# Performance work log

Hardware: AMD Instinct MI355X
Metric: run time of the kernel (lower is better)

Reference implementation:

```python
import jax, jax.numpy as jnp
import numpy as np

C = 512

def conv1x1(x, w, b):
    # x: [B,C,H,W], w: [O,C], b: [O]
    return jnp.einsum('bchw,oc->bohw', x, w) + b[None, :, None, None]

def setup_inputs() -> dict:
    key = jax.random.key(0)
    ks = jax.random.split(key, 7)
    s = 1.0 / np.sqrt(C)
    x = jax.random.normal(ks[0], (8, C, 64, 64), dtype=jnp.float32)
    wq = jax.random.uniform(ks[1], (C, C), jnp.float32, -s, s)
    bq = jax.random.uniform(ks[2], (C,), jnp.float32, -s, s)
    wk = jax.random.uniform(ks[3], (C, C), jnp.float32, -s, s)
    bk = jax.random.uniform(ks[4], (C,), jnp.float32, -s, s)
    wv = jax.random.uniform(ks[5], (C, C), jnp.float32, -s, s)
    bv = jax.random.uniform(ks[6], (C,), jnp.float32, -s, s)
    return {"x": x, "wq": wq, "bq": bq, "wk": wk, "bk": bk, "wv": wv, "bv": bv}

def reference(x, wq, bq, wk, bk, wv, bv):
    B, Cc, H, W = x.shape
    q = conv1x1(x, wq, bq).reshape(B, Cc, H * W)   # [B,C,N]
    k = conv1x1(x, wk, bk).reshape(B, Cc, H * W)   # [B,C,N]
    v = conv1x1(x, wv, bv).reshape(B, Cc, H * W)   # [B,C,N]
    attn = jnp.einsum('bcn,bdn->bcd', q, k)        # q @ k^T over spatial dim -> [B,C,C]
    attn = jax.nn.softmax(attn, axis=-1)
    out = jnp.einsum('bcd,bdn->bcn', attn, v).reshape(B, Cc, H, W)
    return out + x
```

## Files before the change

### kernel.cpp

```cpp
#include <hip/hip_runtime.h>
#include <cstdint>

typedef unsigned short u16;
typedef unsigned int   u32;
typedef _Float16 f16;

typedef __attribute__((ext_vector_type(8))) _Float16 f16x8;
typedef __attribute__((ext_vector_type(4))) float    f32x4;

__device__ __forceinline__ u16 f2h(float f) {
    union { f16 h; u16 u; } c; c.h = (f16)f; return c.u;
}
__device__ __forceinline__ float h2f(u16 u) {
    union { u16 u; f16 h; } c; c.u = u; return (float)c.h;
}

__device__ __forceinline__ void async_copy16(const u16* g, u16* lds) {
    __builtin_amdgcn_global_load_lds(
        (const __attribute__((address_space(1))) void*)g,
        (__attribute__((address_space(3))) void*)lds,
        16, 0, 0);
}

__device__ __forceinline__ void gemm_nt_f16(
    u16* smem, const u16* __restrict__ A, int lda,
    const u16* __restrict__ B, int ldb, int K, f32x4 acc[4][4])
{
    u16* As = smem; u16* Bs = smem + 4096;
    const int t = threadIdx.x, w = t >> 6, lane = t & 63;
    const int srow = lane >> 2;
    const int skc  = (((lane & 3) ^ ((lane >> 3) & 3)) * 8);
    const int ra0 = (w*2+0)*16 + srow, ra1 = (w*2+1)*16 + srow;
    const u16* gA0 = A + (size_t)ra0 * lda + skc;
    const u16* gA1 = A + (size_t)ra1 * lda + skc;
    const u16* gB0 = B + (size_t)ra0 * ldb + skc;
    const u16* gB1 = B + (size_t)ra1 * ldb + skc;
    u16* lA0 = As + (w*2+0)*512; u16* lA1 = As + (w*2+1)*512;
    u16* lB0 = Bs + (w*2+0)*512; u16* lB1 = Bs + (w*2+1)*512;
    const int fr = lane & 15, fq = lane >> 4;
    const int fc = (fq ^ ((fr >> 1) & 3)) * 8;
    const int wm = (w >> 1) * 64, wn = (w & 1) * 64;
    const u16* fA = As + (wm + fr) * 32 + fc;
    const u16* fB = Bs + (wn + fr) * 32 + fc;

    for (int k0 = 0; k0 < K; k0 += 32) {
        async_copy16(gA0 + k0, lA0);
        async_copy16(gA1 + k0, lA1);
        async_copy16(gB0 + k0, lB0);
        async_copy16(gB1 + k0, lB1);
        __syncthreads();
        f16x8 af[4], bf[4];
#pragma unroll
        for (int i = 0; i < 4; i++) af[i] = *(const f16x8*)(fA + i * 512);
#pragma unroll
        for (int i = 0; i < 4; i++) bf[i] = *(const f16x8*)(fB + i * 512);
#pragma unroll
        for (int mi = 0; mi < 4; mi++)
#pragma unroll
            for (int ni = 0; ni < 4; ni++)
                acc[mi][ni] = __builtin_amdgcn_mfma_f32_16x16x32_f16(
                    af[mi], bf[ni], acc[mi][ni], 0, 0, 0);
        __syncthreads();
    }
}

__device__ __forceinline__ void zero_acc(f32x4 acc[4][4]) {
#pragma unroll
    for (int i = 0; i < 4; i++)
#pragma unroll
        for (int j = 0; j < 4; j++) {
            f32x4 z = {0.f, 0.f, 0.f, 0.f};
            acc[i][j] = z;
        }
}

__global__ __launch_bounds__(256) void k_convw(const float* __restrict__ wq,
                                               const float* __restrict__ wk,
                                               u16* __restrict__ Wq2,
                                               u16* __restrict__ Wkh,
                                               float* __restrict__ s)
{
    const int t = blockIdx.x * 256 + threadIdx.x;
    if (t < 4096) s[t] = 0.f;
    const int e = t * 4;
    const int sel = e >> 18;
    const int off = e & 262143;
    const float* src = sel ? wk : wq;
    float4 v = *(const float4*)(src + off);
    ushort4 h;
    h.x = f2h(v.x); h.y = f2h(v.y); h.z = f2h(v.z); h.w = f2h(v.w);
    if (sel == 0) {
        int i = off >> 9, c = off & 511;
        *(ushort4*)(Wq2 + (size_t)i * 1024 + c) = h;
        *(ushort4*)(Wq2 + (size_t)i * 1024 + 512 + c) = h;
    } else {
        *(ushort4*)(Wkh + off) = h;
    }
}

__global__ __launch_bounds__(256) void k_wvt(const float* __restrict__ wv,
                                             u16* __restrict__ WvT)
{
    __shared__ u16 tile[64][70];
    const int t = threadIdx.x;
    const int d0 = blockIdx.y * 64;
    const int c0 = blockIdx.x * 64;
    const int rr = t >> 4, col4 = (t & 15) * 4;
#pragma unroll
    for (int i = 0; i < 4; i++) {
        int row = i * 16 + rr;
        float4 v = *(const float4*)(wv + (size_t)(d0 + row) * 512 + c0 + col4);
        ushort4 h;
        h.x = f2h(v.x); h.y = f2h(v.y); h.z = f2h(v.z); h.w = f2h(v.w);
        *(ushort4*)&tile[row][col4] = h;
    }
    __syncthreads();
#pragma unroll
    for (int i = 0; i < 4; i++) {
        int crow = i * 16 + rr;
        ushort4 o;
        o.x = tile[col4 + 0][crow];
        o.y = tile[col4 + 1][crow];
        o.z = tile[col4 + 2][crow];
        o.w = tile[col4 + 3][crow];
        *(ushort4*)(WvT + (size_t)(c0 + crow) * 512 + d0 + col4) = o;
    }
}

__global__ __launch_bounds__(256) void k_convx(const float* __restrict__ x,
                                               u16* __restrict__ Xh,
                                               u16* __restrict__ XT,
                                               float* __restrict__ s)
{
    __shared__ u16 tile[64][70];
    const int t  = threadIdx.x;
    const int b  = blockIdx.z;
    const int c0 = blockIdx.y * 64;
    const int n0 = blockIdx.x * 64;
    const int rr   = t >> 4;
    const int col4 = (t & 15) * 4;

    const float* src = x + ((size_t)b * 512 + c0) * 4096 + n0;
    u16* xh = Xh + ((size_t)b * 512 + c0) * 4096 + n0;
#pragma unroll
    for (int i = 0; i < 4; i++) {
        int row = i * 16 + rr;
        float4 v = *(const float4*)(src + (size_t)row * 4096 + col4);
        ushort4 h;
        h.x = f2h(v.x); h.y = f2h(v.y); h.z = f2h(v.z); h.w = f2h(v.w);
        *(ushort4*)&tile[row][col4] = h;
        *(ushort4*)(xh + (size_t)row * 4096 + col4) = h;
        float p = v.x + v.y + v.z + v.w;
        p += __shfl_xor(p, 1); p += __shfl_xor(p, 2);
        p += __shfl_xor(p, 4); p += __shfl_xor(p, 8);
        if ((t & 15) == 0) atomicAdd(&s[b * 512 + c0 + row], p);
    }
    __syncthreads();
    u16* dst = XT + ((size_t)b * 4096 + n0) * 512 + c0;
#pragma unroll
    for (int i = 0; i < 4; i++) {
        int nrow = i * 16 + rr;
        ushort4 o;
        o.x = tile[col4 + 0][nrow];
        o.y = tile[col4 + 1][nrow];
        o.z = tile[col4 + 2][nrow];
        o.w = tile[col4 + 3][nrow];
        *(ushort4*)(dst + (size_t)nrow * 512 + col4) = o;
    }
}

__global__ __launch_bounds__(256) void k_gram(const u16* __restrict__ Xh,
                                              float* __restrict__ Gp)
{
    __shared__ u16 smem[8192];
    const int n0 = blockIdx.x * 128;
    const int m0 = blockIdx.y * 128;
    const int bz = blockIdx.z;
    const int b  = bz >> 2, ks = bz & 3;

    const u16* Ap = Xh + (size_t)b * 512 * 4096 + (size_t)m0 * 4096 + ks * 1024;
    const u16* Bp = Xh + (size_t)b * 512 * 4096 + (size_t)n0 * 4096 + ks * 1024;

    f32x4 acc[4][4];
    zero_acc(acc);
    gemm_nt_f16(smem, Ap, 4096, Bp, 4096, 1024, acc);

    const int t = threadIdx.x, w = t >> 6, lane = t & 63;
    const int wm = (w >> 1) * 64, wn = (w & 1) * 64;
    const int cn = lane & 15, cq = lane >> 4;

    float* outp = Gp + ((size_t)(ks * 8 + b) * 512 + m0) * 512 + n0;
#pragma unroll
    for (int mi = 0; mi < 4; mi++)
#pragma unroll
        for (int ni = 0; ni < 4; ni++)
#pragma unroll
            for (int r = 0; r < 4; r++) {
                int m = wm + mi * 16 + cq * 4 + r;
                int n = wn + ni * 16 + cn;
                outp[(size_t)m * 512 + n] = acc[mi][ni][r];
            }
}

__global__ __launch_bounds__(256) void k_gred(const float* __restrict__ Gp,
                                              u16* __restrict__ Ghl)
{
    const size_t idx = ((size_t)blockIdx.x * 256 + threadIdx.x) * 4;
    const size_t st = (size_t)8 * 512 * 512;
    float4 g0 = *(const float4*)(Gp + idx);
    float4 g1 = *(const float4*)(Gp + idx + st);
    float4 g2 = *(const float4*)(Gp + idx + 2 * st);
    float4 g3 = *(const float4*)(Gp + idx + 3 * st);
    float gx = g0.x + g1.x + g2.x + g3.x;
    float gy = g0.y + g1.y + g2.y + g3.y;
    float gz = g0.z + g1.z + g2.z + g3.z;
    float gw = g0.w + g1.w + g2.w + g3.w;
    ushort4 hi, lo;
    hi.x = f2h(gx); lo.x = f2h(gx - h2f(hi.x));
    hi.y = f2h(gy); lo.y = f2h(gy - h2f(hi.y));
    hi.z = f2h(gz); lo.z = f2h(gz - h2f(hi.z));
    hi.w = f2h(gw); lo.w = f2h(gw - h2f(hi.w));
    const size_t row = idx >> 9;
    const int c = (int)(idx & 511);
    *(ushort4*)(Ghl + row * 1024 + c) = hi;
    *(ushort4*)(Ghl + row * 1024 + 512 + c) = lo;
}

__global__ __launch_bounds__(256) void k_uv(const float* __restrict__ wq,
                                            const float* __restrict__ bq,
                                            const float* __restrict__ wk,
                                            const float* __restrict__ s,
                                            float* __restrict__ ubar,
                                            float* __restrict__ vv)
{
    const int b = blockIdx.y;
    const int which = blockIdx.x >> 3;
    const int r0 = (blockIdx.x & 7) * 64;
    const int t = threadIdx.x;
    const int i = r0 + (t >> 2), l4 = t & 3;
    const float* W = which ? wk : wq;
    const float* sb = s + b * 512;
    float acc = 0.f;
#pragma unroll 4
    for (int k = 0; k < 32; k++) {
        int c = k * 16 + l4 * 4;
        float4 w4 = *(const float4*)(W + (size_t)i * 512 + c);
        float4 s4 = *(const float4*)(sb + c);
        acc += w4.x * s4.x + w4.y * s4.y + w4.z * s4.z + w4.w * s4.w;
    }
    acc += __shfl_xor(acc, 1);
    acc += __shfl_xor(acc, 2);
    if (l4 == 0) {
        if (which) vv[b * 512 + i] = acc;
        else       ubar[b * 512 + i] = acc + 4096.0f * bq[i];
    }
}

__global__ __launch_bounds__(256) void k_T(const u16* __restrict__ Wq2,
                                           const u16* __restrict__ Ghl,
                                           u16* __restrict__ Tb)
{
    __shared__ u16 smem[8192];
    const int n0 = blockIdx.x * 128;
    const int m0 = blockIdx.y * 128;
    const int b  = blockIdx.z;

    const u16* Ap = Wq2 + (size_t)m0 * 1024;
    const u16* Bp = Ghl + (size_t)b * 512 * 1024 + (size_t)n0 * 1024;

    f32x4 acc[4][4];
    zero_acc(acc);
    gemm_nt_f16(smem, Ap, 1024, Bp, 1024, 1024, acc);

    const int t = threadIdx.x, w = t >> 6, lane = t & 63;
    const int wm = (w >> 1) * 64, wn = (w & 1) * 64;
    const int cn = lane & 15, cq = lane >> 4;

    u16* outp = Tb + ((size_t)b * 512 + m0) * 512 + n0;
#pragma unroll
    for (int mi = 0; mi < 4; mi++)
#pragma unroll
        for (int ni = 0; ni < 4; ni++)
#pragma unroll
            for (int r = 0; r < 4; r++) {
                int m = wm + mi * 16 + cq * 4 + r;
                int n = wn + ni * 16 + cn;
                outp[(size_t)m * 512 + n] = f2h(acc[mi][ni][r]);
            }
}

__global__ __launch_bounds__(256) void k_S(
    const u16* __restrict__ Tb, const u16* __restrict__ Wkh,
    const float* __restrict__ ubar, const float* __restrict__ vv,
    const float* __restrict__ bq, const float* __restrict__ bk,
    const float* __restrict__ bv,
    u16* __restrict__ P, float* __restrict__ pbv)
{
    __shared__ u16 smem[16896];
    __shared__ float redm[16][4];
    __shared__ float reds[16][4][2];
    u16* As = smem; u16* Bs = smem + 512;

    const int m0 = blockIdx.x * 16;
    const int b  = blockIdx.y;
    const int t = threadIdx.x, w = t >> 6, lane = t & 63;
    const int srow = lane >> 2;
    const int schunk = ((lane & 3) ^ ((srow >> 1) & 3)) * 8;
    const u16* gA = Tb + ((size_t)b * 512 + m0 + srow) * 512 + schunk;
    const int fr = lane & 15, fq = lane >> 4;
    const int fc = (fq ^ ((fr >> 1) & 3)) * 8;

    f32x4 acc[8];
#pragma unroll
    for (int i = 0; i < 8; i++) { f32x4 z = {0.f,0.f,0.f,0.f}; acc[i] = z; }

    for (int k0 = 0; k0 < 512; k0 += 32) {
        if (w == 0) async_copy16(gA + k0, As);
#pragma unroll
        for (int ii = 0; ii < 8; ii++) {
            int rbase = w * 128 + ii * 16;
            async_copy16(Wkh + (size_t)(rbase + srow) * 512 + k0 + schunk,
                         Bs + rbase * 32);
        }
        __syncthreads();
        f16x8 af = *(const f16x8*)(As + fr * 32 + fc);
#pragma unroll
        for (int ni = 0; ni < 8; ni++) {
            f16x8 bf = *(const f16x8*)(Bs + (w * 128 + ni * 16 + fr) * 32 + fc);
            acc[ni] = __builtin_amdgcn_mfma_f32_16x16x32_f16(af, bf, acc[ni], 0, 0, 0);
        }
        __syncthreads();
    }

    const int cn = lane & 15, cq = lane >> 4;
    float ub[4], bqr[4];
#pragma unroll
    for (int r = 0; r < 4; r++) {
        int i = m0 + cq * 4 + r;
        ub[r]  = ubar[b * 512 + i];
        bqr[r] = bq[i];
    }
    float vj[8], bkj[8], bvj[8];
#pragma unroll
    for (int ni = 0; ni < 8; ni++) {
        int j = w * 128 + ni * 16 + cn;
        vj[ni]  = vv[b * 512 + j];
        bkj[ni] = bk[j];
        bvj[ni] = bv[j];
    }
    float sv[8][4], mr[4];
#pragma unroll
    for (int r = 0; r < 4; r++) mr[r] = -1e30f;
#pragma unroll
    for (int ni = 0; ni < 8; ni++)
#pragma unroll
        for (int r = 0; r < 4; r++) {
            sv[ni][r] = acc[ni][r] + ub[r] * bkj[ni] + bqr[r] * vj[ni];
            mr[r] = fmaxf(mr[r], sv[ni][r]);
        }
#pragma unroll
    for (int r = 0; r < 4; r++)
        for (int o = 1; o < 16; o <<= 1) mr[r] = fmaxf(mr[r], __shfl_xor(mr[r], o));
    if (cn == 0) {
#pragma unroll
        for (int r = 0; r < 4; r++) redm[cq * 4 + r][w] = mr[r];
    }
    __syncthreads();
#pragma unroll
    for (int r = 0; r < 4; r++) {
        int row = cq * 4 + r;
        mr[r] = fmaxf(fmaxf(redm[row][0], redm[row][1]),
                      fmaxf(redm[row][2], redm[row][3]));
    }
    float e[8][4], se[4], sebv[4];
#pragma unroll
    for (int r = 0; r < 4; r++) { se[r] = 0.f; sebv[r] = 0.f; }
#pragma unroll
    for (int ni = 0; ni < 8; ni++)
#pragma unroll
        for (int r = 0; r < 4; r++) {
            float ev = __expf(sv[ni][r] - mr[r]);
            e[ni][r] = ev;
            se[r]   += ev;
            sebv[r] += ev * bvj[ni];
        }
#pragma unroll
    for (int r = 0; r < 4; r++)
        for (int o = 1; o < 16; o <<= 1) {
            se[r]   += __shfl_xor(se[r], o);
            sebv[r] += __shfl_xor(sebv[r], o);
        }
    if (cn == 0) {
#pragma unroll
        for (int r = 0; r < 4; r++) {
            reds[cq * 4 + r][w][0] = se[r];
            reds[cq * 4 + r][w][1] = sebv[r];
        }
    }
    __syncthreads();
#pragma unroll
    for (int r = 0; r < 4; r++) {
        int row = cq * 4 + r;
        float S  = reds[row][0][0] + reds[row][1][0] + reds[row][2][0] + reds[row][3][0];
        float SB = reds[row][0][1] + reds[row][1][1] + reds[row][2][1] + reds[row][3][1];
        float inv = 1.0f / S;
#pragma unroll
        for (int ni = 0; ni < 8; ni++)
            P[((size_t)b * 512 + m0 + row) * 512 + w * 128 + ni * 16 + cn] =
                f2h(e[ni][r] * inv);
        if (w == 0 && cn == 0) pbv[b * 512 + m0 + row] = SB * inv;
    }
}

__global__ __launch_bounds__(256) void k_M(const u16* __restrict__ P,
                                           const u16* __restrict__ WvT,
                                           u16* __restrict__ M2)
{
    __shared__ u16 smem[8192];
    const int n0 = blockIdx.x * 128;
    const int m0 = blockIdx.y * 128;
    const int b  = blockIdx.z;

    const u16* Ap = P + (size_t)b * 512 * 512 + (size_t)m0 * 512;
    const u16* Bp = WvT + (size_t)n0 * 512;

    f32x4 acc[4][4];
    zero_acc(acc);
    gemm_nt_f16(smem, Ap, 512, Bp, 512, 512, acc);

    const int t = threadIdx.x, w = t >> 6, lane = t & 63;
    const int wm = (w >> 1) * 64, wn = (w & 1) * 64;
    const int cn = lane & 15, cq = lane >> 4;

    u16* outp = M2 + ((size_t)b * 512 + m0) * 512 + n0;
#pragma unroll
    for (int mi = 0; mi < 4; mi++)
#pragma unroll
        for (int ni = 0; ni < 4; ni++)
#pragma unroll
            for (int r = 0; r < 4; r++) {
                int m = wm + mi * 16 + cq * 4 + r;
                int n = wn + ni * 16 + cn;
                outp[(size_t)m * 512 + n] = f2h(acc[mi][ni][r]);
            }
}

__global__ __launch_bounds__(256) void k_out(const u16* __restrict__ M2,
                                             const u16* __restrict__ XT,
                                             const u16* __restrict__ Xh,
                                             const float* __restrict__ pbv,
                                             float* __restrict__ out)
{
    __shared__ u16 smem[8192];
    const int n0 = blockIdx.x * 128;
    const int m0 = blockIdx.y * 128;
    const int b  = blockIdx.z;

    const u16* Ap = M2 + (size_t)b * 512 * 512 + (size_t)m0 * 512;
    const u16* Bp = XT + (size_t)b * 4096 * 512 + (size_t)n0 * 512;

    f32x4 acc[4][4];
    zero_acc(acc);
    gemm_nt_f16(smem, Ap, 512, Bp, 512, 512, acc);

    const int t = threadIdx.x, w = t >> 6, lane = t & 63;
    const int wm = (w >> 1) * 64, wn = (w & 1) * 64;
    const int cn = lane & 15, cq = lane >> 4;

#pragma unroll
    for (int mi = 0; mi < 4; mi++)
#pragma unroll
        for (int ni = 0; ni < 4; ni++)
#pragma unroll
            for (int r = 0; r < 4; r++) {
                int m = m0 + wm + mi * 16 + cq * 4 + r;
                int n = n0 + wn + ni * 16 + cn;
                size_t idx = ((size_t)b * 512 + m) * 4096 + n;
                out[idx] = acc[mi][ni][r] + pbv[b * 512 + m] + h2f(Xh[idx]);
            }
}

extern "C" void kernel_launch(void* const* d_in, const int* in_sizes, int n_in,
                              void* d_out, int out_size, void* d_ws, size_t ws_size,
                              hipStream_t stream)
{
    const float* x  = (const float*)d_in[0];
    const float* wq = (const float*)d_in[1];
    const float* bq = (const float*)d_in[2];
    const float* wk = (const float*)d_in[3];
    const float* bk = (const float*)d_in[4];
    const float* wv = (const float*)d_in[5];
    const float* bv = (const float*)d_in[6];
    float* out = (float*)d_out;

    char* ws = (char*)d_ws;
    u16*   Wq2  = (u16*)(ws);
    u16*   Wkh  = (u16*)(ws + 1048576);
    u16*   WvT  = (u16*)(ws + 1572864);
    float* s    = (float*)(ws + 2097152);
    float* ubar = (float*)(ws + 2113536);
    float* vv   = (float*)(ws + 2129920);
    float* pbv  = (float*)(ws + 2146304);
    u16*   Xh   = (u16*)(ws + 2162688);
    u16*   XT   = (u16*)(ws + 35717120);
    float* Gp   = (float*)(ws + 69271552);
    u16*   Ghl  = (u16*)(ws + 102825984);
    u16*   Tb   = (u16*)(ws + 111214592);
    u16*   P    = (u16*)(ws + 115408896);
    u16*   M2   = (u16*)(ws + 119603200);

    k_convw<<<dim3(512), dim3(256), 0, stream>>>(wq, wk, Wq2, Wkh, s);
    k_wvt<<<dim3(8, 8), dim3(256), 0, stream>>>(wv, WvT);
    k_convx<<<dim3(64, 8, 8), dim3(256), 0, stream>>>(x, Xh, XT, s);
    k_gram<<<dim3(4, 4, 32), dim3(256), 0, stream>>>(Xh, Gp);
    k_gred<<<dim3(2048), dim3(256), 0, stream>>>(Gp, Ghl);
    k_uv<<<dim3(16, 8), dim3(256), 0, stream>>>(wq, bq, wk, s, ubar, vv);
    k_T<<<dim3(4, 4, 8), dim3(256), 0, stream>>>(Wq2, Ghl, Tb);
    k_S<<<dim3(32, 8), dim3(256), 0, stream>>>(Tb, Wkh, ubar, vv, bq, bk, bv, P, pbv);
    k_M<<<dim3(4, 4, 8), dim3(256), 0, stream>>>(P, WvT, M2);
    k_out<<<dim3(32, 4, 8), dim3(256), 0, stream>>>(M2, XT, Xh, pbv, out);
}
```

Baseline: 267.3 us.

## Double-buffer GEMM LDS tiles, merge prep and uv kernels, halve gram split-K

The shared NT GEMM helper and the k_S loop are converted to a two-buffer LDS pipeline, so the next k-slice's async global-to-LDS copy is issued before computing on the current slice. This hides load latency and removes one barrier per iteration, but doubles LDS per block (32 KB for most GEMMs, about 66 KB for k_S), which may lower occupancy. The weight-conversion and Wv-transpose kernels are merged into one launch, and the ubar/vv kernel is folded into the Gram-reduction kernel. The Gram split-K factor drops from 4 to 2, which halves the partial-sum traffic but also halves that kernel's grid.

```diff
diff --git a/kernel.cpp b/kernel.cpp
--- a/kernel.cpp
+++ b/kernel.cpp
@@ -26,7 +26,6 @@
     u16* smem, const u16* __restrict__ A, int lda,
     const u16* __restrict__ B, int ldb, int K, f32x4 acc[4][4])
 {
-    u16* As = smem; u16* Bs = smem + 4096;
     const int t = threadIdx.x, w = t >> 6, lane = t & 63;
     const int srow = lane >> 2;
     const int skc  = (((lane & 3) ^ ((lane >> 3) & 3)) * 8);
@@ -35,33 +34,46 @@
     const u16* gA1 = A + (size_t)ra1 * lda + skc;
     const u16* gB0 = B + (size_t)ra0 * ldb + skc;
     const u16* gB1 = B + (size_t)ra1 * ldb + skc;
-    u16* lA0 = As + (w*2+0)*512; u16* lA1 = As + (w*2+1)*512;
-    u16* lB0 = Bs + (w*2+0)*512; u16* lB1 = Bs + (w*2+1)*512;
+    const int lo0 = (w*2+0)*512, lo1 = (w*2+1)*512;
     const int fr = lane & 15, fq = lane >> 4;
     const int fc = (fq ^ ((fr >> 1) & 3)) * 8;
     const int wm = (w >> 1) * 64, wn = (w & 1) * 64;
-    const u16* fA = As + (wm + fr) * 32 + fc;
-    const u16* fB = Bs + (wn + fr) * 32 + fc;
-
-    for (int k0 = 0; k0 < K; k0 += 32) {
-        async_copy16(gA0 + k0, lA0);
-        async_copy16(gA1 + k0, lA1);
-        async_copy16(gB0 + k0, lB0);
-        async_copy16(gB1 + k0, lB1);
+    const int fAo = (wm + fr) * 32 + fc;
+    const int fBo = 4096 + (wn + fr) * 32 + fc;
+
+#define STAGE_NT(buf, k0)                                          \
+    {   u16* base = smem + (buf) * 8192;                           \
+        async_copy16(gA0 + (k0), base + lo0);                      \
+        async_copy16(gA1 + (k0), base + lo1);                      \
+        async_copy16(gB0 + (k0), base + 4096 + lo0);               \
+        async_copy16(gB1 + (k0), base + 4096 + lo1);  }
+
+#define COMPUTE_NT(buf)                                            \
+    {   const u16* bb = smem + (buf) * 8192;                       \
+        f16x8 af[4], bf[4];                                        \
+        _Pragma("unroll")                                          \
+        for (int i = 0; i < 4; i++) af[i] = *(const f16x8*)(bb + fAo + i * 512); \
+        _Pragma("unroll")                                          \
+        for (int i = 0; i < 4; i++) bf[i] = *(const f16x8*)(bb + fBo + i * 512); \
+        _Pragma("unroll")                                          \
+        for (int mi = 0; mi < 4; mi++)                             \
+            _Pragma("unroll")                                      \
+            for (int ni = 0; ni < 4; ni++)                         \
+                acc[mi][ni] = __builtin_amdgcn_mfma_f32_16x16x32_f16( \
+                    af[mi], bf[ni], acc[mi][ni], 0, 0, 0);  }
+
+    STAGE_NT(0, 0);
+    __syncthreads();
+    int cur = 0;
+    for (int k0 = 32; k0 < K; k0 += 32) {
+        STAGE_NT(cur ^ 1, k0);
+        COMPUTE_NT(cur);
         __syncthreads();
-        f16x8 af[4], bf[4];
-#pragma unroll
-        for (int i = 0; i < 4; i++) af[i] = *(const f16x8*)(fA + i * 512);
-#pragma unroll
-        for (int i = 0; i < 4; i++) bf[i] = *(const f16x8*)(fB + i * 512);
-#pragma unroll
-        for (int mi = 0; mi < 4; mi++)
-#pragma unroll
-            for (int ni = 0; ni < 4; ni++)
-                acc[mi][ni] = __builtin_amdgcn_mfma_f32_16x16x32_f16(
-                    af[mi], bf[ni], acc[mi][ni], 0, 0, 0);
-        __syncthreads();
-    }
+        cur ^= 1;
+    }
+    COMPUTE_NT(cur);
+#undef STAGE_NT
+#undef COMPUTE_NT
 }
 
 __device__ __forceinline__ void zero_acc(f32x4 acc[4][4]) {
@@ -74,56 +86,57 @@
         }
 }
 
-__global__ __launch_bounds__(256) void k_convw(const float* __restrict__ wq,
-                                               const float* __restrict__ wk,
-                                               u16* __restrict__ Wq2,
-                                               u16* __restrict__ Wkh,
-                                               float* __restrict__ s)
-{
-    const int t = blockIdx.x * 256 + threadIdx.x;
-    if (t < 4096) s[t] = 0.f;
-    const int e = t * 4;
-    const int sel = e >> 18;
-    const int off = e & 262143;
-    const float* src = sel ? wk : wq;
-    float4 v = *(const float4*)(src + off);
-    ushort4 h;
-    h.x = f2h(v.x); h.y = f2h(v.y); h.z = f2h(v.z); h.w = f2h(v.w);
-    if (sel == 0) {
-        int i = off >> 9, c = off & 511;
-        *(ushort4*)(Wq2 + (size_t)i * 1024 + c) = h;
-        *(ushort4*)(Wq2 + (size_t)i * 1024 + 512 + c) = h;
-    } else {
-        *(ushort4*)(Wkh + off) = h;
-    }
-}
-
-__global__ __launch_bounds__(256) void k_wvt(const float* __restrict__ wv,
-                                             u16* __restrict__ WvT)
-{
-    __shared__ u16 tile[64][70];
-    const int t = threadIdx.x;
-    const int d0 = blockIdx.y * 64;
-    const int c0 = blockIdx.x * 64;
-    const int rr = t >> 4, col4 = (t & 15) * 4;
-#pragma unroll
-    for (int i = 0; i < 4; i++) {
-        int row = i * 16 + rr;
-        float4 v = *(const float4*)(wv + (size_t)(d0 + row) * 512 + c0 + col4);
+__global__ __launch_bounds__(256) void k_prep(const float* __restrict__ wq,
+                                              const float* __restrict__ wk,
+                                              const float* __restrict__ wv,
+                                              u16* __restrict__ Wq2,
+                                              u16* __restrict__ Wkh,
+                                              u16* __restrict__ WvT,
+                                              float* __restrict__ s)
+{
+    if (blockIdx.x < 512) {
+        const int t = blockIdx.x * 256 + threadIdx.x;
+        if (t < 4096) s[t] = 0.f;
+        const int e = t * 4;
+        const int sel = e >> 18;
+        const int off = e & 262143;
+        const float* src = sel ? wk : wq;
+        float4 v = *(const float4*)(src + off);
         ushort4 h;
         h.x = f2h(v.x); h.y = f2h(v.y); h.z = f2h(v.z); h.w = f2h(v.w);
-        *(ushort4*)&tile[row][col4] = h;
-    }
-    __syncthreads();
-#pragma unroll
-    for (int i = 0; i < 4; i++) {
-        int crow = i * 16 + rr;
-        ushort4 o;
-        o.x = tile[col4 + 0][crow];
-        o.y = tile[col4 + 1][crow];
-        o.z = tile[col4 + 2][crow];
-        o.w = tile[col4 + 3][crow];
-        *(ushort4*)(WvT + (size_t)(c0 + crow) * 512 + d0 + col4) = o;
+        if (sel == 0) {
+            int i = off >> 9, c = off & 511;
+            *(ushort4*)(Wq2 + (size_t)i * 1024 + c) = h;
+            *(ushort4*)(Wq2 + (size_t)i * 1024 + 512 + c) = h;
+        } else {
+            *(ushort4*)(Wkh + off) = h;
+        }
+    } else {
+        __shared__ u16 tile[64][70];
+        const int bx = blockIdx.x - 512;
+        const int t = threadIdx.x;
+        const int d0 = (bx >> 3) * 64;
+        const int c0 = (bx & 7) * 64;
+        const int rr = t >> 4, col4 = (t & 15) * 4;
+#pragma unroll
+        for (int i = 0; i < 4; i++) {
+            int row = i * 16 + rr;
+            float4 v = *(const float4*)(wv + (size_t)(d0 + row) * 512 + c0 + col4);
+            ushort4 h;
+            h.x = f2h(v.x); h.y = f2h(v.y); h.z = f2h(v.z); h.w = f2h(v.w);
+            *(ushort4*)&tile[row][col4] = h;
+        }
+        __syncthreads();
+#pragma unroll
+        for (int i = 0; i < 4; i++) {
+            int crow = i * 16 + rr;
+            ushort4 o;
+            o.x = tile[col4 + 0][crow];
+            o.y = tile[col4 + 1][crow];
+            o.z = tile[col4 + 2][crow];
+            o.w = tile[col4 + 3][crow];
+            *(ushort4*)(WvT + (size_t)(c0 + crow) * 512 + d0 + col4) = o;
+        }
     }
 }
 
@@ -172,18 +185,18 @@
 __global__ __launch_bounds__(256) void k_gram(const u16* __restrict__ Xh,
                                               float* __restrict__ Gp)
 {
-    __shared__ u16 smem[8192];
+    __shared__ u16 smem[2][8192];
     const int n0 = blockIdx.x * 128;
     const int m0 = blockIdx.y * 128;
     const int bz = blockIdx.z;
-    const int b  = bz >> 2, ks = bz & 3;
-
-    const u16* Ap = Xh + (size_t)b * 512 * 4096 + (size_t)m0 * 4096 + ks * 1024;
-    const u16* Bp = Xh + (size_t)b * 512 * 4096 + (size_t)n0 * 4096 + ks * 1024;
+    const int b  = bz >> 1, ks = bz & 1;
+
+    const u16* Ap = Xh + (size_t)b * 512 * 4096 + (size_t)m0 * 4096 + ks * 2048;
+    const u16* Bp = Xh + (size_t)b * 512 * 4096 + (size_t)n0 * 4096 + ks * 2048;
 
     f32x4 acc[4][4];
     zero_acc(acc);
-    gemm_nt_f16(smem, Ap, 4096, Bp, 4096, 1024, acc);
+    gemm_nt_f16(&smem[0][0], Ap, 4096, Bp, 4096, 2048, acc);
 
     const int t = threadIdx.x, w = t >> 6, lane = t & 63;
     const int wm = (w >> 1) * 64, wn = (w & 1) * 64;
@@ -203,18 +216,22 @@
 }
 
 __global__ __launch_bounds__(256) void k_gred(const float* __restrict__ Gp,
-                                              u16* __restrict__ Ghl)
+                                              u16* __restrict__ Ghl,
+                                              const float* __restrict__ wq,
+                                              const float* __restrict__ bq,
+                                              const float* __restrict__ wk,
+                                              const float* __restrict__ s,
+                                              float* __restrict__ ubar,
+                                              float* __restrict__ vv)
 {
     const size_t idx = ((size_t)blockIdx.x * 256 + threadIdx.x) * 4;
     const size_t st = (size_t)8 * 512 * 512;
     float4 g0 = *(const float4*)(Gp + idx);
     float4 g1 = *(const float4*)(Gp + idx + st);
-    float4 g2 = *(const float4*)(Gp + idx + 2 * st);
-    float4 g3 = *(const float4*)(Gp + idx + 3 * st);
-    float gx = g0.x + g1.x + g2.x + g3.x;
-    float gy = g0.y + g1.y + g2.y + g3.y;
-    float gz = g0.z + g1.z + g2.z + g3.z;
-    float gw = g0.w + g1.w + g2.w + g3.w;
+    float gx = g0.x + g1.x;
+    float gy = g0.y + g1.y;
+    float gz = g0.z + g1.z;
+    float gw = g0.w + g1.w;
     ushort4 hi, lo;
     hi.x = f2h(gx); lo.x = f2h(gx - h2f(hi.x));
     hi.y = f2h(gy); lo.y = f2h(gy - h2f(hi.y));
@@ -224,35 +241,30 @@
     const int c = (int)(idx & 511);
     *(ushort4*)(Ghl + row * 1024 + c) = hi;
     *(ushort4*)(Ghl + row * 1024 + 512 + c) = lo;
-}
-
-__global__ __launch_bounds__(256) void k_uv(const float* __restrict__ wq,
-                                            const float* __restrict__ bq,
-                                            const float* __restrict__ wk,
-                                            const float* __restrict__ s,
-                                            float* __restrict__ ubar,
-                                            float* __restrict__ vv)
-{
-    const int b = blockIdx.y;
-    const int which = blockIdx.x >> 3;
-    const int r0 = (blockIdx.x & 7) * 64;
-    const int t = threadIdx.x;
-    const int i = r0 + (t >> 2), l4 = t & 3;
-    const float* W = which ? wk : wq;
-    const float* sb = s + b * 512;
-    float acc = 0.f;
+
+    if (blockIdx.x < 128) {
+        const int b = blockIdx.x >> 4;
+        const int sub = blockIdx.x & 15;
+        const int which = sub >> 3;
+        const int r0 = (sub & 7) * 64;
+        const int t = threadIdx.x;
+        const int i = r0 + (t >> 2), l4 = t & 3;
+        const float* W = which ? wk : wq;
+        const float* sb = s + b * 512;
+        float acc = 0.f;
 #pragma unroll 4
-    for (int k = 0; k < 32; k++) {
-        int c = k * 16 + l4 * 4;
-        float4 w4 = *(const float4*)(W + (size_t)i * 512 + c);
-        float4 s4 = *(const float4*)(sb + c);
-        acc += w4.x * s4.x + w4.y * s4.y + w4.z * s4.z + w4.w * s4.w;
-    }
-    acc += __shfl_xor(acc, 1);
-    acc += __shfl_xor(acc, 2);
-    if (l4 == 0) {
-        if (which) vv[b * 512 + i] = acc;
-        else       ubar[b * 512 + i] = acc + 4096.0f * bq[i];
+        for (int k = 0; k < 32; k++) {
+            int c2 = k * 16 + l4 * 4;
+            float4 w4 = *(const float4*)(W + (size_t)i * 512 + c2);
+            float4 s4 = *(const float4*)(sb + c2);
+            acc += w4.x * s4.x + w4.y * s4.y + w4.z * s4.z + w4.w * s4.w;
+        }
+        acc += __shfl_xor(acc, 1);
+        acc += __shfl_xor(acc, 2);
+        if (l4 == 0) {
+            if (which) vv[b * 512 + i] = acc;
+            else       ubar[b * 512 + i] = acc + 4096.0f * bq[i];
+        }
     }
 }
 
@@ -260,7 +272,7 @@
                                            const u16* __restrict__ Ghl,
                                            u16* __restrict__ Tb)
 {
-    __shared__ u16 smem[8192];
+    __shared__ u16 smem[2][8192];
     const int n0 = blockIdx.x * 128;
     const int m0 = blockIdx.y * 128;
     const int b  = blockIdx.z;
@@ -270,7 +282,7 @@
 
     f32x4 acc[4][4];
     zero_acc(acc);
-    gemm_nt_f16(smem, Ap, 1024, Bp, 1024, 1024, acc);
+    gemm_nt_f16(&smem[0][0], Ap, 1024, Bp, 1024, 1024, acc);
 
     const int t = threadIdx.x, w = t >> 6, lane = t & 63;
     const int wm = (w >> 1) * 64, wn = (w & 1) * 64;
@@ -296,10 +308,9 @@
     const float* __restrict__ bv,
     u16* __restrict__ P, float* __restrict__ pbv)
 {
-    __shared__ u16 smem[16896];
+    __shared__ u16 smem[2][16896];
     __shared__ float redm[16][4];
     __shared__ float reds[16][4][2];
-    u16* As = smem; u16* Bs = smem + 512;
 
     const int m0 = blockIdx.x * 16;
     const int b  = blockIdx.y;
@@ -314,23 +325,36 @@
 #pragma unroll
     for (int i = 0; i < 8; i++) { f32x4 z = {0.f,0.f,0.f,0.f}; acc[i] = z; }
 
-    for (int k0 = 0; k0 < 512; k0 += 32) {
-        if (w == 0) async_copy16(gA + k0, As);
-#pragma unroll
-        for (int ii = 0; ii < 8; ii++) {
-            int rbase = w * 128 + ii * 16;
-            async_copy16(Wkh + (size_t)(rbase + srow) * 512 + k0 + schunk,
-                         Bs + rbase * 32);
-        }
+#define STAGE_S(buf, k0)                                                     \
+    {   u16* As = smem[buf]; u16* Bs = smem[buf] + 512;                      \
+        if (w == 0) async_copy16(gA + (k0), As);                             \
+        _Pragma("unroll")                                                    \
+        for (int ii = 0; ii < 8; ii++) {                                     \
+            int rbase = w * 128 + ii * 16;                                   \
+            async_copy16(Wkh + (size_t)(rbase + srow) * 512 + (k0) + schunk, \
+                         Bs + rbase * 32);  }  }
+
+#define COMPUTE_S(buf)                                                       \
+    {   const u16* As = smem[buf]; const u16* Bs = smem[buf] + 512;          \
+        f16x8 af = *(const f16x8*)(As + fr * 32 + fc);                       \
+        _Pragma("unroll")                                                    \
+        for (int ni = 0; ni < 8; ni++) {                                     \
+            f16x8 bf = *(const f16x8*)(Bs + (w * 128 + ni * 16 + fr) * 32 + fc); \
+            acc[ni] = __builtin_amdgcn_mfma_f32_16x16x32_f16(af, bf, acc[ni], 0, 0, 0); \
+        }  }
+
+    STAGE_S(0, 0);
+    __syncthreads();
+    int cur = 0;
+    for (int k0 = 32; k0 < 512; k0 += 32) {
+        STAGE_S(cur ^ 1, k0);
+        COMPUTE_S(cur);
         __syncthreads();
-        f16x8 af = *(const f16x8*)(As + fr * 32 + fc);
-#pragma unroll
-        for (int ni = 0; ni < 8; ni++) {
-            f16x8 bf = *(const f16x8*)(Bs + (w * 128 + ni * 16 + fr) * 32 + fc);
-            acc[ni] = __builtin_amdgcn_mfma_f32_16x16x32_f16(af, bf, acc[ni], 0, 0, 0);
-        }
-        __syncthreads();
-    }
+        cur ^= 1;
+    }
+    COMPUTE_S(cur);
+#undef STAGE_S
+#undef COMPUTE_S
 
     const int cn = lane & 15, cq = lane >> 4;
     float ub[4], bqr[4];
@@ -416,7 +440,7 @@
                                            const u16* __restrict__ WvT,
                                            u16* __restrict__ M2)
 {
-    __shared__ u16 smem[8192];
+    __shared__ u16 smem[2][8192];
     const int n0 = blockIdx.x * 128;
     const int m0 = blockIdx.y * 128;
     const int b  = blockIdx.z;
@@ -426,7 +450,7 @@
 
     f32x4 acc[4][4];
     zero_acc(acc);
-    gemm_nt_f16(smem, Ap, 512, Bp, 512, 512, acc);
+    gemm_nt_f16(&smem[0][0], Ap, 512, Bp, 512, 512, acc);
 
     const int t = threadIdx.x, w = t >> 6, lane = t & 63;
     const int wm = (w >> 1) * 64, wn = (w & 1) * 64;
@@ -451,7 +475,7 @@
                                              const float* __restrict__ pbv,
                                              float* __restrict__ out)
 {
-    __shared__ u16 smem[8192];
+    __shared__ u16 smem[2][8192];
     const int n0 = blockIdx.x * 128;
     const int m0 = blockIdx.y * 128;
     const int b  = blockIdx.z;
@@ -461,7 +485,7 @@
 
     f32x4 acc[4][4];
     zero_acc(acc);
-    gemm_nt_f16(smem, Ap, 512, Bp, 512, 512, acc);
+    gemm_nt_f16(&smem[0][0], Ap, 512, Bp, 512, 512, acc);
 
     const int t = threadIdx.x, w = t >> 6, lane = t & 63;
     const int wm = (w >> 1) * 64, wn = (w & 1) * 64;
@@ -504,17 +528,15 @@
     u16*   Xh   = (u16*)(ws + 2162688);
     u16*   XT   = (u16*)(ws + 35717120);
     float* Gp   = (float*)(ws + 69271552);
-    u16*   Ghl  = (u16*)(ws + 102825984);
-    u16*   Tb   = (u16*)(ws + 111214592);
-    u16*   P    = (u16*)(ws + 115408896);
-    u16*   M2   = (u16*)(ws + 119603200);
-
-    k_convw<<<dim3(512), dim3(256), 0, stream>>>(wq, wk, Wq2, Wkh, s);
-    k_wvt<<<dim3(8, 8), dim3(256), 0, stream>>>(wv, WvT);
+    u16*   Ghl  = (u16*)(ws + 86048768);
+    u16*   Tb   = (u16*)(ws + 94437376);
+    u16*   P    = (u16*)(ws + 98631680);
+    u16*   M2   = (u16*)(ws + 102825984);
+
+    k_prep<<<dim3(576), dim3(256), 0, stream>>>(wq, wk, wv, Wq2, Wkh, WvT, s);
     k_convx<<<dim3(64, 8, 8), dim3(256), 0, stream>>>(x, Xh, XT, s);
-    k_gram<<<dim3(4, 4, 32), dim3(256), 0, stream>>>(Xh, Gp);
-    k_gred<<<dim3(2048), dim3(256), 0, stream>>>(Gp, Ghl);
-    k_uv<<<dim3(16, 8), dim3(256), 0, stream>>>(wq, bq, wk, s, ubar, vv);
+    k_gram<<<dim3(4, 4, 16), dim3(256), 0, stream>>>(Xh, Gp);
+    k_gred<<<dim3(2048), dim3(256), 0, stream>>>(Gp, Ghl, wq, bq, wk, s, ubar, vv);
     k_T<<<dim3(4, 4, 8), dim3(256), 0, stream>>>(Wq2, Ghl, Tb);
     k_S<<<dim3(32, 8), dim3(256), 0, stream>>>(Tb, Wkh, ubar, vv, bq, bk, bv, P, pbv);
     k_M<<<dim3(4, 4, 8), dim3(256), 0, stream>>>(P, WvT, M2);
```

Result: slower. 279.4 us (+4.5%).
